# Optimization experiments

Measured on AMD Instinct MI355X. Metric: run time of the kernel, lower is better.

Reference implementation:

```python
import jax, jax.numpy as jnp
import numpy as np

SQ, B, H = 2048, 1, 4096
NP, HN, MQG = 32, 128, 2          # query heads, head_dim, kv groups
ROT = HN // 2                      # rotary dim = 64 (partial rotary)
NORM = float(np.sqrt(HN))


def apply_rope(x, rope):
    # x: [sq, b, nh, hn]; rope: [sq, 1, ROT//2, 2] (cos, sin)
    sq, b, nh, hn = x.shape
    rot = rope.shape[-2] * 2
    xr, xp = x[..., :rot], x[..., rot:]
    xs = xr.reshape(sq, b, nh, rot // 2, 2)
    rc = rope[:sq].reshape(sq, -1, 1, rot // 2, 2)
    o0 = xs[..., 0] * rc[..., 0] - xs[..., 1] * rc[..., 1]
    o1 = xs[..., 1] * rc[..., 0] + xs[..., 0] * rc[..., 1]
    out = jnp.stack([o0, o1], -1).reshape(sq, b, nh, rot)
    return jnp.concatenate([out, xp], axis=-1)


def setup_inputs() -> dict:
    key = jax.random.key(0)
    k0, k1, k2, k3 = jax.random.split(key, 4)
    qkv_dim = NP * HN + 2 * MQG * HN  # 4608
    hidden_states = jax.random.normal(k0, (SQ, B, H), jnp.float32) * 0.02
    Wqkv = jax.random.normal(k1, (qkv_dim, H), jnp.float32) * 0.02
    bqkv = jax.random.normal(k2, (qkv_dim,), jnp.float32) * 0.02
    Wdense = jax.random.normal(k3, (H, NP * HN), jnp.float32) * 0.02
    # rope cache [sq, 1, ROT//2, 2]
    pos = jnp.arange(SQ, dtype=jnp.float32)
    inv = 1.0 / (10000.0 ** (jnp.arange(0, ROT, 2, dtype=jnp.float32) / ROT))
    ang = pos[:, None] * inv[None, :]
    rotary_pos_emb = jnp.stack([jnp.cos(ang), jnp.sin(ang)], -1)[:, None, :, :]
    # additive causal mask [b, 1, sq, sq]
    causal = jnp.tril(jnp.ones((SQ, SQ), bool))
    attention_mask = jnp.broadcast_to(
        jnp.where(causal, 0.0, -1e9).astype(jnp.float32), (B, 1, SQ, SQ))
    return dict(hidden_states=hidden_states, Wqkv=Wqkv, bqkv=bqkv,
                Wdense=Wdense, rotary_pos_emb=rotary_pos_emb,
                attention_mask=attention_mask)


def reference(hidden_states, Wqkv, bqkv, Wdense, rotary_pos_emb, attention_mask):
    sq, b, _ = hidden_states.shape
    mixed = hidden_states @ Wqkv.T + bqkv            # [sq, b, 4608]
    qd, kvd = NP * HN, MQG * HN
    q = mixed[..., :qd].reshape(sq, b, NP, HN)
    k = mixed[..., qd:qd + kvd].reshape(sq, b, MQG, HN)
    v = mixed[..., qd + kvd:].reshape(sq, b, MQG, HN)
    q = apply_rope(q, rotary_pos_emb)
    k = apply_rope(k, rotary_pos_emb)
    # -> [b, heads, sq, hn]
    q = q.transpose(1, 2, 0, 3)
    k = k.transpose(1, 2, 0, 3)
    v = v.transpose(1, 2, 0, 3)
    # MQA grouping: q [b, g, n_rep, sq, hn]; kv kept at [b, g, sq, hn]
    n_rep = NP // MQG
    qg = q.reshape(b, MQG, n_rep, sq, HN)
    scores = jnp.einsum('bgrqd,bgkd->bgrqk', qg, k) / NORM
    scores = scores + attention_mask[:, None]        # [b,1,1,sq,sq] broadcast
    probs = jax.nn.softmax(scores.astype(jnp.float32), axis=-1).astype(q.dtype)
    ctx = jnp.einsum('bgrqk,bgkd->bgrqd', probs, v)  # [b, g, n_rep, sq, hn]
    ctx = ctx.reshape(b, NP, sq, HN).transpose(0, 2, 1, 3).reshape(b, sq, NP * HN)
    out = ctx @ Wdense.T                             # [b, sq, H]
    return out
```

## Files before the change

kernel.cpp:

```cpp
#include <hip/hip_runtime.h>
#include <stdint.h>

#define SQL 2048
#define HID 4096
#define NHEADS 32
#define HDSZ 128
#define QKVD 4608
#define QDIM 4096

typedef unsigned short u16;
typedef __attribute__((ext_vector_type(8))) short short8;
typedef __attribute__((ext_vector_type(4))) float f32x4;

#define AS1(p) ((__attribute__((address_space(1))) void*)(p))
#define AS3(p) ((__attribute__((address_space(3))) void*)(p))

__device__ __forceinline__ float bf2f(u16 u) {
  return __uint_as_float(((uint32_t)u) << 16);
}
__device__ __forceinline__ u16 f2bf(float f) {
  uint32_t x = __float_as_uint(f);
  x += 0x7fffu + ((x >> 16) & 1u);
  return (u16)(x >> 16);
}

__global__ void k_cvt(const float* __restrict__ in, u16* __restrict__ out, int n8) {
  int i = blockIdx.x * blockDim.x + threadIdx.x;
  int stride = gridDim.x * blockDim.x;
  for (; i < n8; i += stride) {
    const float4* p = reinterpret_cast<const float4*>(in) + (size_t)i * 2;
    float4 a = p[0], b = p[1];
    short8 o;
    o[0] = (short)f2bf(a.x); o[1] = (short)f2bf(a.y);
    o[2] = (short)f2bf(a.z); o[3] = (short)f2bf(a.w);
    o[4] = (short)f2bf(b.x); o[5] = (short)f2bf(b.y);
    o[6] = (short)f2bf(b.z); o[7] = (short)f2bf(b.w);
    reinterpret_cast<short8*>(out)[i] = o;
  }
}

template<int MODE>
__global__ __launch_bounds__(256, 2)
void k_gemm(const u16* __restrict__ A, const u16* __restrict__ B,
            const float* __restrict__ bias,
            u16* __restrict__ qbuf, u16* __restrict__ kbuf, u16* __restrict__ vtbuf,
            float* __restrict__ outf)
{
  __shared__ __align__(16) u16 ldsA[128 * 64];
  __shared__ __align__(16) u16 ldsB[128 * 64];
  const int tid = threadIdx.x;
  const int wid = tid >> 6, lane = tid & 63;
  const int l15 = lane & 15, lg = lane >> 4;
  const int m0 = blockIdx.y * 128, n0 = blockIdx.x * 128;
  const int wr = wid >> 1, wc = wid & 1;

  f32x4 acc[4][4] = {};

  const int srow = lane >> 3;
  const int skb  = (((lane & 7) ^ srow) << 4);
  const size_t rowbytes = (size_t)HID * 2;

  for (int t = 0; t < HID / 64; ++t) {
    __syncthreads();
    const char* Ab = (const char*)A + (size_t)m0 * rowbytes + (size_t)t * 128;
    const char* Bb = (const char*)B + (size_t)n0 * rowbytes + (size_t)t * 128;
#pragma unroll
    for (int i = 0; i < 4; ++i) {
      int seg = i * 4 + wid;
      int row = seg * 8 + srow;
      __builtin_amdgcn_global_load_lds(AS1(Ab + (size_t)row * rowbytes + skb),
                                       AS3(ldsA + seg * 512), 16, 0, 0);
      __builtin_amdgcn_global_load_lds(AS1(Bb + (size_t)row * rowbytes + skb),
                                       AS3(ldsB + seg * 512), 16, 0, 0);
    }
    __syncthreads();
#pragma unroll
    for (int kc = 0; kc < 2; ++kc) {
      short8 af[4], bfr[4];
#pragma unroll
      for (int mi = 0; mi < 4; ++mi) {
        int row = wr * 64 + mi * 16 + l15;
        int kb = (kc * 64 + lg * 16) ^ ((row & 7) << 4);
        af[mi] = *reinterpret_cast<const short8*>((const char*)ldsA + row * 128 + kb);
      }
#pragma unroll
      for (int ni = 0; ni < 4; ++ni) {
        int row = wc * 64 + ni * 16 + l15;
        int kb = (kc * 64 + lg * 16) ^ ((row & 7) << 4);
        bfr[ni] = *reinterpret_cast<const short8*>((const char*)ldsB + row * 128 + kb);
      }
#pragma unroll
      for (int mi = 0; mi < 4; ++mi)
#pragma unroll
        for (int ni = 0; ni < 4; ++ni)
          acc[mi][ni] = __builtin_amdgcn_mfma_f32_16x16x32_bf16(af[mi], bfr[ni], acc[mi][ni], 0, 0, 0);
    }
  }

#pragma unroll
  for (int mi = 0; mi < 4; ++mi) {
#pragma unroll
    for (int ni = 0; ni < 4; ++ni) {
      int row0 = m0 + wr * 64 + mi * 16 + lg * 4;
      int col  = n0 + wc * 64 + ni * 16 + l15;
      if (MODE == 0) {
        float bv = bias[col];
#pragma unroll
        for (int j = 0; j < 4; ++j) {
          float v = acc[mi][ni][j] + bv;
          u16 hb = f2bf(v);
          int r = row0 + j;
          if (col < QDIM) {
            int hh = col >> 7, d = col & 127;
            qbuf[((size_t)hh * SQL + r) * HDSZ + d] = hb;
          } else if (col < QDIM + 256) {
            int c2 = col - QDIM; int g = c2 >> 7, d = c2 & 127;
            kbuf[((size_t)g * SQL + r) * HDSZ + d] = hb;
          } else {
            int c2 = col - QDIM - 256; int g = c2 >> 7, d = c2 & 127;
            vtbuf[((size_t)g * HDSZ + d) * SQL + r] = hb;
          }
        }
      } else {
#pragma unroll
        for (int j = 0; j < 4; ++j)
          outf[(size_t)(row0 + j) * QDIM + col] = acc[mi][ni][j];
      }
    }
  }
}

__global__ void k_rope(u16* __restrict__ qbuf, u16* __restrict__ kbuf,
                       const float* __restrict__ rope) {
  int idx = blockIdx.x * blockDim.x + threadIdx.x;
  if (idx >= SQL * 34 * 32) return;
  int p = idx & 31;
  int hh = (idx >> 5) % 34;
  int s = idx / (34 * 32);
  float c  = rope[s * 64 + p * 2 + 0];
  float sn = rope[s * 64 + p * 2 + 1];
  u16* base = (hh < 32) ? (qbuf + ((size_t)hh * SQL + s) * HDSZ)
                        : (kbuf + ((size_t)(hh - 32) * SQL + s) * HDSZ);
  u16* pp = base + 2 * p;
  uint32_t packed = *reinterpret_cast<uint32_t*>(pp);
  float x0 = bf2f((u16)(packed & 0xffff));
  float x1 = bf2f((u16)(packed >> 16));
  float o0 = x0 * c - x1 * sn;
  float o1 = x1 * c + x0 * sn;
  *reinterpret_cast<uint32_t*>(pp) = (uint32_t)f2bf(o0) | ((uint32_t)f2bf(o1) << 16);
}

template<int SPLIT>
__global__ __launch_bounds__(64)
void k_attn(const u16* __restrict__ qbuf, const u16* __restrict__ kbuf,
            const u16* __restrict__ vtbuf,
            u16* __restrict__ part, float2* __restrict__ mlbuf,
            u16* __restrict__ ctx)
{
  __shared__ __align__(16) u16 pls[32 * 72];
  const int lane = threadIdx.x;
  const int l15 = lane & 15, lg = lane >> 4;
  const int h = blockIdx.x;
  const int g = h >> 4;
  int qi, ci;
  if (SPLIT) {
    int p = blockIdx.y;
    if (p < 32)      { qi = 32 + p;  ci = 0; }
    else if (p < 64) { qi = 95 - p;  ci = 1; }
    else             { qi = 95 - p;  ci = 0; }
  } else {
    qi = (int)gridDim.y - 1 - (int)blockIdx.y;
    ci = 0;
  }
  const int q0 = qi * 32;
  const int E  = q0 + 32;
  const int c0 = SPLIT ? ci * 1024 : 0;
  const int c1 = SPLIT ? min(c0 + 1024, E) : E;
  const float inv_norm = 0.08838834764831845f;

  short8 aq[2][4];
#pragma unroll
  for (int rt = 0; rt < 2; ++rt) {
    const u16* qp = qbuf + ((size_t)h * SQL + q0 + rt * 16 + l15) * HDSZ + lg * 8;
#pragma unroll
    for (int kc = 0; kc < 4; ++kc)
      aq[rt][kc] = *reinterpret_cast<const short8*>(qp + kc * 32);
  }
  f32x4 o[2][8] = {};
  float mrow[2][4], lrow[2][4];
#pragma unroll
  for (int rt = 0; rt < 2; ++rt)
#pragma unroll
    for (int j = 0; j < 4; ++j) { mrow[rt][j] = -__builtin_inff(); lrow[rt][j] = 0.f; }

  for (int j0 = c0; j0 < c1; j0 += 64) {
    short8 bk[4][4];
    const u16* kp = kbuf + ((size_t)g * SQL + j0 + l15) * HDSZ + lg * 8;
#pragma unroll
    for (int kt = 0; kt < 4; ++kt)
#pragma unroll
      for (int kc = 0; kc < 4; ++kc)
        bk[kt][kc] = *reinterpret_cast<const short8*>(kp + (size_t)kt * 16 * HDSZ + kc * 32);

    f32x4 s[2][4] = {};
    __builtin_amdgcn_s_setprio(1);
#pragma unroll
    for (int kc = 0; kc < 4; ++kc)
#pragma unroll
      for (int rt = 0; rt < 2; ++rt)
#pragma unroll
        for (int kt = 0; kt < 4; ++kt)
          s[rt][kt] = __builtin_amdgcn_mfma_f32_16x16x32_bf16(aq[rt][kc], bk[kt][kc], s[rt][kt], 0, 0, 0);
    __builtin_amdgcn_s_setprio(0);

    short8 bv[8][2];
    const u16* vp = vtbuf + ((size_t)g * HDSZ + l15) * SQL + j0 + lg * 8;
#pragma unroll
    for (int df = 0; df < 8; ++df)
#pragma unroll
      for (int kc2 = 0; kc2 < 2; ++kc2)
        bv[df][kc2] = *reinterpret_cast<const short8*>(vp + (size_t)df * 16 * SQL + kc2 * 32);

    const bool domask = (j0 + 63 > q0);
    float al[2][4];
#pragma unroll
    for (int rt = 0; rt < 2; ++rt) {
#pragma unroll
      for (int j = 0; j < 4; ++j) {
        int row = q0 + rt * 16 + lg * 4 + j;
        float v[4];
        if (domask) {
#pragma unroll
          for (int kt = 0; kt < 4; ++kt)
            v[kt] = (j0 + kt * 16 + l15 > row) ? -1e30f : s[rt][kt][j] * inv_norm;
        } else {
#pragma unroll
          for (int kt = 0; kt < 4; ++kt)
            v[kt] = s[rt][kt][j] * inv_norm;
        }
        float rm = fmaxf(fmaxf(v[0], v[1]), fmaxf(v[2], v[3]));
        rm = fmaxf(rm, __shfl_xor(rm, 1));
        rm = fmaxf(rm, __shfl_xor(rm, 2));
        rm = fmaxf(rm, __shfl_xor(rm, 4));
        rm = fmaxf(rm, __shfl_xor(rm, 8));
        float mn = fmaxf(mrow[rt][j], rm);
        float a = __expf(mrow[rt][j] - mn);
        mrow[rt][j] = mn;
        float p[4], ps = 0.f;
#pragma unroll
        for (int kt = 0; kt < 4; ++kt) { p[kt] = __expf(v[kt] - mn); ps += p[kt]; }
        ps += __shfl_xor(ps, 1);
        ps += __shfl_xor(ps, 2);
        ps += __shfl_xor(ps, 4);
        ps += __shfl_xor(ps, 8);
        lrow[rt][j] = lrow[rt][j] * a + ps;
        al[rt][j] = a;
        int rl = rt * 16 + lg * 4 + j;
#pragma unroll
        for (int kt = 0; kt < 4; ++kt)
          pls[rl * 72 + kt * 16 + l15] = f2bf(p[kt]);
      }
    }
    asm volatile("s_waitcnt lgkmcnt(0)" ::: "memory");

    short8 ap[2][2];
#pragma unroll
    for (int rt = 0; rt < 2; ++rt)
#pragma unroll
      for (int kc2 = 0; kc2 < 2; ++kc2)
        ap[rt][kc2] = *reinterpret_cast<const short8*>(&pls[(rt * 16 + l15) * 72 + kc2 * 32 + lg * 8]);

    __builtin_amdgcn_s_setprio(1);
#pragma unroll
    for (int rt = 0; rt < 2; ++rt) {
#pragma unroll
      for (int df = 0; df < 8; ++df) {
        f32x4 t = o[rt][df];
        t[0] *= al[rt][0]; t[1] *= al[rt][1]; t[2] *= al[rt][2]; t[3] *= al[rt][3];
        t = __builtin_amdgcn_mfma_f32_16x16x32_bf16(ap[rt][0], bv[df][0], t, 0, 0, 0);
        t = __builtin_amdgcn_mfma_f32_16x16x32_bf16(ap[rt][1], bv[df][1], t, 0, 0, 0);
        o[rt][df] = t;
      }
    }
    __builtin_amdgcn_s_setprio(0);
  }

  if (SPLIT) {
    const int pid = (h * 64 + qi) * 2 + ci;
    u16* pp = part + (size_t)pid * 32 * 128;
#pragma unroll
    for (int rt = 0; rt < 2; ++rt) {
#pragma unroll
      for (int j = 0; j < 4; ++j) {
        float inv_l = 1.0f / lrow[rt][j];
        int rl = rt * 16 + lg * 4 + j;
#pragma unroll
        for (int df = 0; df < 8; ++df)
          pp[rl * 128 + df * 16 + l15] = f2bf(o[rt][df][j] * inv_l);
        if (l15 == 0)
          mlbuf[pid * 32 + rl] = make_float2(mrow[rt][j], lrow[rt][j]);
      }
    }
  } else {
#pragma unroll
    for (int rt = 0; rt < 2; ++rt) {
#pragma unroll
      for (int j = 0; j < 4; ++j) {
        float inv_l = 1.0f / lrow[rt][j];
        int row = q0 + rt * 16 + lg * 4 + j;
        u16* cp = ctx + (size_t)row * QDIM + h * HDSZ;
#pragma unroll
        for (int df = 0; df < 8; ++df)
          cp[df * 16 + l15] = f2bf(o[rt][df][j] * inv_l);
      }
    }
  }
}

__global__ __launch_bounds__(256)
void k_merge(const u16* __restrict__ part, const float2* __restrict__ mlbuf,
             u16* __restrict__ ctx)
{
  int idx = blockIdx.x * 256 + threadIdx.x;
  int d8  = idx & 15;
  int row = (idx >> 4) & 2047;
  int h   = idx >> 15;
  int qi = row >> 5, rl = row & 31;
  int pid0 = (h * 64 + qi) * 2;
  float2 ml0 = mlbuf[pid0 * 32 + rl];
  short8 p0 = *reinterpret_cast<const short8*>(part + ((size_t)pid0 * 32 + rl) * 128 + d8 * 8);
  short8 p1 = p0;
  float w0 = ml0.y, w1 = 0.f;
  if (qi >= 32) {
    float2 ml1 = mlbuf[(pid0 + 1) * 32 + rl];
    p1 = *reinterpret_cast<const short8*>(part + ((size_t)(pid0 + 1) * 32 + rl) * 128 + d8 * 8);
    float ms = fmaxf(ml0.x, ml1.x);
    w0 = ml0.y * __expf(ml0.x - ms);
    w1 = ml1.y * __expf(ml1.x - ms);
  }
  float inv_s = 1.0f / (w0 + w1);
  w0 *= inv_s; w1 *= inv_s;
  short8 o;
#pragma unroll
  for (int e = 0; e < 8; ++e)
    o[e] = (short)f2bf(w0 * bf2f((u16)p0[e]) + w1 * bf2f((u16)p1[e]));
  *reinterpret_cast<short8*>(ctx + (size_t)row * QDIM + h * 128 + d8 * 8) = o;
}


#define WS_PART 73400320ull
#define WS_ML   106954752ull
#define WS_NEED 108003328ull

extern "C" void kernel_launch(void* const* d_in, const int* in_sizes, int n_in,
                              void* d_out, int out_size, void* d_ws, size_t ws_size,
                              hipStream_t stream) {
  const float* hs     = (const float*)d_in[0];
  const float* wqkv   = (const float*)d_in[1];
  const float* bqkv   = (const float*)d_in[2];
  const float* wdense = (const float*)d_in[3];
  const float* rope   = (const float*)d_in[4];
  char* ws = (char*)d_ws;
  u16* hid_b = (u16*)(ws + 0);
  u16* w_b   = (u16*)(ws + 16777216);
  u16* qb    = (u16*)(ws + 54525952);
  u16* kb    = (u16*)(ws + 71303168);
  u16* vtb   = (u16*)(ws + 72351744);
  u16* part  = (u16*)(ws + WS_PART);
  float2* ml = (float2*)(ws + WS_ML);
  u16* ctx   = hid_b;
  float* outf = (float*)d_out;

  k_cvt<<<2048, 256, 0, stream>>>(hs,   hid_b, SQL * HID / 8);
  k_cvt<<<2048, 256, 0, stream>>>(wqkv, w_b,   QKVD * HID / 8);
  k_gemm<0><<<dim3(QKVD / 128, SQL / 128), 256, 0, stream>>>(
      hid_b, w_b, bqkv, qb, kb, vtb, nullptr);
  k_rope<<<(SQL * 34 * 32) / 256, 256, 0, stream>>>(qb, kb, rope);
  k_cvt<<<2048, 256, 0, stream>>>(wdense, w_b, QDIM * HID / 8);
  if (ws_size >= WS_NEED) {
    k_attn<1><<<dim3(NHEADS, 96), 64, 0, stream>>>(qb, kb, vtb, part, ml, nullptr);
    k_merge<<<(NHEADS * SQL * 16) / 256, 256, 0, stream>>>(part, ml, ctx);
  } else {
    k_attn<0><<<dim3(NHEADS, SQL / 32), 64, 0, stream>>>(qb, kb, vtb, nullptr, nullptr, ctx);
  }
  k_gemm<1><<<dim3(QDIM / 128, SQL / 128), 256, 0, stream>>>(
      ctx, w_b, nullptr, nullptr, nullptr, nullptr, outf);
}
```

Measured before the change: 369.7 us.

## Split causal attention KV range into 256-key chunks for finer load balance

Replaces the two-way 1024-key split of the attention work with variable splitting into 256-key chunks, so each query tile of 32 rows gets one block per chunk (288 blocks per head). Single-chunk tiles write context directly, and the merge kernel now combines up to eight partials using log-sum-exp weights. The aim is more even per-block work and more blocks in flight for the causal triangle. In exchange it writes more partial output and adds merge traffic and a larger workspace requirement.

```diff
diff --git a/kernel.cpp b/kernel.cpp
--- a/kernel.cpp
+++ b/kernel.cpp
@@ -150,6 +150,9 @@
   *reinterpret_cast<uint32_t*>(pp) = (uint32_t)f2bf(o0) | ((uint32_t)f2bf(o1) << 16);
 }
 
+#define CHK 256
+#define PPH 288
+
 template<int SPLIT>
 __global__ __launch_bounds__(64)
 void k_attn(const u16* __restrict__ qbuf, const u16* __restrict__ kbuf,
@@ -162,20 +165,26 @@
   const int l15 = lane & 15, lg = lane >> 4;
   const int h = blockIdx.x;
   const int g = h >> 4;
-  int qi, ci;
+  int qi, ci, nchk = 1;
   if (SPLIT) {
-    int p = blockIdx.y;
-    if (p < 32)      { qi = 32 + p;  ci = 0; }
-    else if (p < 64) { qi = 95 - p;  ci = 1; }
-    else             { qi = 95 - p;  ci = 0; }
+    int off = blockIdx.y, b = 0;
+#pragma unroll
+    for (int bb = 0; bb < 8; ++bb) {
+      int bs = 8 * (bb + 1);
+      if (off < bs) { b = bb; break; }
+      off -= bs;
+    }
+    nchk = b + 1;
+    qi = (b << 3) + off / nchk;
+    ci = off % nchk;
   } else {
     qi = (int)gridDim.y - 1 - (int)blockIdx.y;
     ci = 0;
   }
   const int q0 = qi * 32;
   const int E  = q0 + 32;
-  const int c0 = SPLIT ? ci * 1024 : 0;
-  const int c1 = SPLIT ? min(c0 + 1024, E) : E;
+  const int c0 = SPLIT ? ci * CHK : 0;
+  const int c1 = SPLIT ? min(c0 + CHK, E) : E;
   const float inv_norm = 0.08838834764831845f;
 
   short8 aq[2][4];
@@ -285,8 +294,8 @@
     __builtin_amdgcn_s_setprio(0);
   }
 
-  if (SPLIT) {
-    const int pid = (h * 64 + qi) * 2 + ci;
+  if (SPLIT && nchk > 1) {
+    const int pid = h * PPH + blockIdx.y;
     u16* pp = part + (size_t)pid * 32 * 128;
 #pragma unroll
     for (int rt = 0; rt < 2; ++rt) {
@@ -323,34 +332,45 @@
 {
   int idx = blockIdx.x * 256 + threadIdx.x;
   int d8  = idx & 15;
-  int row = (idx >> 4) & 2047;
-  int h   = idx >> 15;
-  int qi = row >> 5, rl = row & 31;
-  int pid0 = (h * 64 + qi) * 2;
-  float2 ml0 = mlbuf[pid0 * 32 + rl];
-  short8 p0 = *reinterpret_cast<const short8*>(part + ((size_t)pid0 * 32 + rl) * 128 + d8 * 8);
-  short8 p1 = p0;
-  float w0 = ml0.y, w1 = 0.f;
-  if (qi >= 32) {
-    float2 ml1 = mlbuf[(pid0 + 1) * 32 + rl];
-    p1 = *reinterpret_cast<const short8*>(part + ((size_t)(pid0 + 1) * 32 + rl) * 128 + d8 * 8);
-    float ms = fmaxf(ml0.x, ml1.x);
-    w0 = ml0.y * __expf(ml0.x - ms);
-    w1 = ml1.y * __expf(ml1.x - ms);
-  }
-  float inv_s = 1.0f / (w0 + w1);
-  w0 *= inv_s; w1 *= inv_s;
+  int r   = idx >> 4;
+  int h   = r / 1792;
+  int rr  = r - h * 1792;
+  int qi  = 8 + (rr >> 5);
+  int rl  = rr & 31;
+  int row = qi * 32 + rl;
+  int b   = qi >> 3;
+  int nc  = b + 1;
+  int base = h * PPH + 4 * b * (b + 1) + (qi & 7) * nc;
+
+  float m[8], l[8], M = -__builtin_inff();
+  for (int c = 0; c < nc; ++c) {
+    float2 ml = mlbuf[(base + c) * 32 + rl];
+    m[c] = ml.x; l[c] = ml.y;
+    M = fmaxf(M, ml.x);
+  }
+  float w[8], W = 0.f;
+  for (int c = 0; c < nc; ++c) { w[c] = l[c] * __expf(m[c] - M); W += w[c]; }
+  float invW = 1.0f / W;
+
+  float acc[8] = {};
+  for (int c = 0; c < nc; ++c) {
+    short8 p = *reinterpret_cast<const short8*>(
+        part + ((size_t)(base + c) * 32 + rl) * 128 + d8 * 8);
+    float wc = w[c] * invW;
+#pragma unroll
+    for (int e = 0; e < 8; ++e)
+      acc[e] += wc * bf2f((u16)p[e]);
+  }
   short8 o;
 #pragma unroll
-  for (int e = 0; e < 8; ++e)
-    o[e] = (short)f2bf(w0 * bf2f((u16)p0[e]) + w1 * bf2f((u16)p1[e]));
+  for (int e = 0; e < 8; ++e) o[e] = (short)f2bf(acc[e]);
   *reinterpret_cast<short8*>(ctx + (size_t)row * QDIM + h * 128 + d8 * 8) = o;
 }
 
 
 #define WS_PART 73400320ull
-#define WS_ML   106954752ull
-#define WS_NEED 108003328ull
+#define WS_ML   148897792ull
+#define WS_NEED 151257088ull
 
 extern "C" void kernel_launch(void* const* d_in, const int* in_sizes, int n_in,
                               void* d_out, int out_size, void* d_ws, size_t ws_size,
@@ -378,8 +398,8 @@
   k_rope<<<(SQL * 34 * 32) / 256, 256, 0, stream>>>(qb, kb, rope);
   k_cvt<<<2048, 256, 0, stream>>>(wdense, w_b, QDIM * HID / 8);
   if (ws_size >= WS_NEED) {
-    k_attn<1><<<dim3(NHEADS, 96), 64, 0, stream>>>(qb, kb, vtb, part, ml, nullptr);
-    k_merge<<<(NHEADS * SQL * 16) / 256, 256, 0, stream>>>(part, ml, ctx);
+    k_attn<1><<<dim3(NHEADS, PPH), 64, 0, stream>>>(qb, kb, vtb, part, ml, ctx);
+    k_merge<<<(NHEADS * 1792 * 16) / 256, 256, 0, stream>>>(part, ml, ctx);
   } else {
     k_attn<0><<<dim3(NHEADS, SQL / 32), 64, 0, stream>>>(qb, kb, vtb, nullptr, nullptr, ctx);
   }
```

Measured after the change: 409.2 us. 1.11x slower.
